# Performance work log

Hardware: AMD Instinct MI355X
Metric: run time of the kernel (lower is better)

The kernel has to match this reference:

```python
import jax, jax.numpy as jnp
import numpy as np

NEG = -9e15


def make_adj_mask(edge_index, n):
    # dense mask: 0 on edges and diagonal, -9e15 elsewhere (vectorized version of the source loop)
    A = jnp.full((n, n), NEG, dtype=jnp.float32)
    A = jnp.where(jnp.eye(n, dtype=bool), 0.0, A)
    A = A.at[edge_index[0], edge_index[1]].set(0.0)
    return A


def gat_layer(x, W, b, a_left, a_right, mask, num_heads, concat, alpha=0.2):
    n = x.shape[0]
    feats = (x @ W + b).reshape(n, num_heads, -1)           # [n, h, c]
    s_src = jnp.einsum('nhc,ch->nh', feats, a_left)          # score of source (column) node
    s_tgt = jnp.einsum('nhc,ch->nh', feats, a_right)         # score of target (row) node
    # all_scores[i, j, h] = s_src[j, h] + s_tgt[i, h]
    scores = jax.nn.leaky_relu(s_src[None, :, :] + s_tgt[:, None, :], alpha)
    scores = jnp.transpose(scores, (2, 0, 1)) + mask         # [h, n, n]
    attn = jax.nn.softmax(scores, axis=2)
    out = jnp.einsum('hij,jhc->ihc', attn, feats)            # [n, h, c]
    if concat:
        return out.reshape(n, -1)
    return out.mean(axis=1)


def setup_inputs() -> dict:
    key = jax.random.key(0)
    ks = jax.random.split(key, 10)
    N, F, H, C_HID, N_CLS, E = 4096, 512, 8, 64, 7, 65536
    c_ph = C_HID // H  # 8 per head
    s = 0.05
    return {
        'x': jax.random.normal(ks[0], (N, F), dtype=jnp.float32),
        'edge_index': jax.random.randint(ks[1], (2, E), 0, N, dtype=jnp.int32),
        'W1': jax.random.normal(ks[2], (F, C_HID), dtype=jnp.float32) * s,
        'b1': jnp.zeros((C_HID,), dtype=jnp.float32),
        'a_left1': jax.random.normal(ks[3], (c_ph, H), dtype=jnp.float32) * s,
        'a_right1': jax.random.normal(ks[4], (c_ph, H), dtype=jnp.float32) * s,
        'W2': jax.random.normal(ks[5], (C_HID, N_CLS), dtype=jnp.float32) * s,
        'b2': jnp.zeros((N_CLS,), dtype=jnp.float32),
        'a_left2': jax.random.normal(ks[6], (N_CLS, 1), dtype=jnp.float32) * s,
        'a_right2': jax.random.normal(ks[7], (N_CLS, 1), dtype=jnp.float32) * s,
    }


def reference(x, edge_index, W1, b1, a_left1, a_right1, W2, b2, a_left2, a_right2):
    n = x.shape[0]
    mask = make_adj_mask(edge_index, n)
    h1 = gat_layer(x, W1, b1, a_left1, a_right1, mask, num_heads=8, concat=True)
    h1 = jax.nn.elu(h1)
    out = gat_layer(h1, W2, b2, a_left2, a_right2, mask, num_heads=1, concat=False)
    return out
```

## Files before the change

kernel.cpp:

```cpp
#include <hip/hip_runtime.h>
#include <math.h>

#define NNODES 4096
#define WPR 128
#define FDIM 512
#define CHID 64
#define NHEAD 8
#define NCLS 7
#define MAXD 4096

typedef short bf16x8 __attribute__((ext_vector_type(8)));
typedef float f32x4  __attribute__((ext_vector_type(4)));

static __device__ inline short f2bf(float f) {
    union { float f; unsigned u; } v; v.f = f;
    unsigned r = v.u + 0x7fffu + ((v.u >> 16) & 1u);
    return (short)(r >> 16);
}

__global__ void k_init(unsigned int* __restrict__ adj, const float* __restrict__ W1,
                       short* __restrict__ Bp) {
    int bid = blockIdx.x;
    if (bid < 2048) {
        int idx = bid * 256 + threadIdx.x;
        int row = idx >> 7;
        int w = idx & (WPR - 1);
        adj[idx] = (w == (row >> 5)) ? (1u << (row & 31)) : 0u;
    } else {
        int t = (bid - 2048) * 256 + threadIdx.x;
        int j = t & 7, l = (t >> 3) & 63, w = (t >> 9) & 3, kb = t >> 11;
        Bp[t] = f2bf(W1[(kb * 32 + (l >> 4) * 8 + j) * 64 + (w * 16 + (l & 15))]);
    }
}

__global__ void k_adj_edges(const int* __restrict__ ei, unsigned int* __restrict__ adj, int E) {
    int e = blockIdx.x * blockDim.x + threadIdx.x;
    if (e >= E) return;
    int r = ei[e];
    int c = ei[E + e];
    atomicOr(&adj[r * WPR + (c >> 5)], 1u << (c & 31));
}

__global__ void __launch_bounds__(256) k_gemm1(const float* __restrict__ x, const short* __restrict__ Bp,
                                               const float* __restrict__ b, const float* __restrict__ al,
                                               const float* __restrict__ ar,
                                               const unsigned int* __restrict__ adj,
                                               float* __restrict__ feats, float* __restrict__ s1,
                                               int* __restrict__ nbrL, int* __restrict__ degA) {
    const int w = threadIdx.x >> 6, l = threadIdx.x & 63;
    const int row0 = blockIdx.x * 16;
    const int arow = row0 + (l & 15);
    const int koff = (l >> 4) * 8;
    f32x4 acc = {0.f, 0.f, 0.f, 0.f};
    const bf16x8* bp = (const bf16x8*)Bp;
    #pragma unroll
    for (int kb = 0; kb < 16; ++kb) {
        const float* ap = &x[arow * FDIM + kb * 32 + koff];
        const float4 a0 = *(const float4*)ap;
        const float4 a1 = *(const float4*)(ap + 4);
        bf16x8 af = { f2bf(a0.x), f2bf(a0.y), f2bf(a0.z), f2bf(a0.w),
                      f2bf(a1.x), f2bf(a1.y), f2bf(a1.z), f2bf(a1.w) };
        bf16x8 bfr = bp[(kb * 4 + w) * 64 + l];
        acc = __builtin_amdgcn_mfma_f32_16x16x32_bf16(af, bfr, acc, 0, 0, 0);
    }
    const int col = w * 16 + (l & 15);
    const int r0 = row0 + (l >> 4) * 4;
    const float bias = b[col];
    const int c = col & 7, h = col >> 3;
    const float vl = al[c * NHEAD + h];
    const float vr = ar[c * NHEAD + h];
    #pragma unroll
    for (int r = 0; r < 4; ++r) {
        float fv = acc[r] + bias;
        feats[(r0 + r) * CHID + col] = fv;
        float ps = fv * vl, pt = fv * vr;
        ps += __shfl_xor(ps, 1); ps += __shfl_xor(ps, 2); ps += __shfl_xor(ps, 4);
        pt += __shfl_xor(pt, 1); pt += __shfl_xor(pt, 2); pt += __shfl_xor(pt, 4);
        if ((l & 7) == 0) {
            s1[(r0 + r) * 16 + h] = ps;
            s1[(r0 + r) * 16 + 8 + h] = pt;
        }
    }
    for (int q = 0; q < 4; ++q) {
        const int i = row0 + w * 4 + q;
        const unsigned w0 = adj[i * WPR + 2 * l];
        const unsigned w1 = adj[i * WPR + 2 * l + 1];
        const int c0 = __popc(w0), c1 = __popc(w1);
        const int tot = c0 + c1;
        int v = tot;
        #pragma unroll
        for (int d = 1; d < 64; d <<= 1) {
            int t = __shfl_up(v, d);
            if (l >= d) v += t;
        }
        const int excl = v - tot;
        int base = i * MAXD + excl;
        unsigned bits = w0; int p = 0;
        while (bits) { int bb = __ffs(bits) - 1; bits &= bits - 1; nbrL[base + p++] = l * 64 + bb; }
        base += c0;
        bits = w1; p = 0;
        while (bits) { int bb = __ffs(bits) - 1; bits &= bits - 1; nbrL[base + p++] = l * 64 + 32 + bb; }
        if (l == 63) degA[i] = v;
    }
}

__global__ void __launch_bounds__(256) k_attn1(const int* __restrict__ nbrL, const int* __restrict__ degA,
                                               const float* __restrict__ feats,
                                               const float* __restrict__ s1,
                                               const float* __restrict__ W2,
                                               const float* __restrict__ b2,
                                               const float* __restrict__ al2,
                                               const float* __restrict__ ar2,
                                               float* __restrict__ feats2,
                                               float* __restrict__ s2) {
    const int w = threadIdx.x >> 6, l = threadIdx.x & 63;
    const int i = blockIdx.x * 4 + w;
    const int h = l >> 3;
    const int nn = degA[i];
    const float stgt = s1[i * 16 + 8 + h];
    float den = 0.f, acc = 0.f;
    for (int k0 = 0; k0 < nn; k0 += 64) {
        const int rem = nn - k0;
        const int cmax = rem < 64 ? rem : 64;
        const int jv = nbrL[i * MAXD + k0 + (l < cmax ? l : 0)];
        for (int k = 0; k < cmax; ++k) {
            const int j = __shfl(jv, k);
            float sc = s1[j * 16 + h] + stgt;
            sc = sc > 0.f ? sc : 0.2f * sc;
            const float p = __expf(sc);
            den += p;
            acc = fmaf(p, feats[j * CHID + l], acc);
        }
    }
    const float o = acc / den;
    const float h1v = o > 0.f ? o : (__expf(o) - 1.f);
    float t[NCLS];
    #pragma unroll
    for (int c2 = 0; c2 < NCLS; ++c2) {
        float p = h1v * W2[l * NCLS + c2];
        p += __shfl_xor(p, 1);  p += __shfl_xor(p, 2);  p += __shfl_xor(p, 4);
        p += __shfl_xor(p, 8);  p += __shfl_xor(p, 16); p += __shfl_xor(p, 32);
        t[c2] = p + b2[c2];
    }
    if (l == 0) {
        float ss = 0.f, st = 0.f;
        #pragma unroll
        for (int c2 = 0; c2 < NCLS; ++c2) {
            ss = fmaf(t[c2], al2[c2], ss);
            st = fmaf(t[c2], ar2[c2], st);
        }
        #pragma unroll
        for (int c2 = 0; c2 < NCLS; ++c2) feats2[i * 8 + c2] = t[c2];
        feats2[i * 8 + 7] = 0.f;
        s2[i * 2] = ss;
        s2[i * 2 + 1] = st;
    }
}

__global__ void __launch_bounds__(256) k_attn2(const int* __restrict__ nbrL, const int* __restrict__ degA,
                                               const float* __restrict__ feats2,
                                               const float* __restrict__ s2,
                                               float* __restrict__ out) {
    const int w = threadIdx.x >> 6, l = threadIdx.x & 63;
    const int i = blockIdx.x * 4 + w;
    const int nn = degA[i];
    const int c = l & 7;
    const float stgt = s2[i * 2 + 1];
    float den = 0.f, acc = 0.f;
    for (int k0 = 0; k0 < nn; k0 += 64) {
        const int rem = nn - k0;
        const int cmax = rem < 64 ? rem : 64;
        const int jv = nbrL[i * MAXD + k0 + (l < cmax ? l : 0)];
        for (int k = 0; k < cmax; ++k) {
            const int j = __shfl(jv, k);
            float sc = s2[j * 2] + stgt;
            sc = sc > 0.f ? sc : 0.2f * sc;
            const float p = __expf(sc);
            den += p;
            acc = fmaf(p, feats2[j * 8 + c], acc);
        }
    }
    if (l < NCLS) out[i * NCLS + l] = acc / den;
}

extern "C" void kernel_launch(void* const* d_in, const int* in_sizes, int n_in,
                              void* d_out, int out_size, void* d_ws, size_t ws_size,
                              hipStream_t stream) {
    const float* x   = (const float*)d_in[0];
    const int*   ei  = (const int*)d_in[1];
    const float* W1  = (const float*)d_in[2];
    const float* b1  = (const float*)d_in[3];
    const float* al1 = (const float*)d_in[4];
    const float* ar1 = (const float*)d_in[5];
    const float* W2  = (const float*)d_in[6];
    const float* b2  = (const float*)d_in[7];
    const float* al2 = (const float*)d_in[8];
    const float* ar2 = (const float*)d_in[9];
    float* out = (float*)d_out;
    int E = in_sizes[1] / 2;

    char* ws = (char*)d_ws;
    unsigned int* adj = (unsigned int*)ws;
    short* Bp     = (short*)(ws + (2u << 20));
    float* feats1 = (float*)(ws + (3u << 20));
    float* s1     = (float*)(ws + (4u << 20));
    float* feats2 = (float*)(ws + (5u << 20));
    float* s2     = (float*)(ws + (6u << 20));
    int*   degA   = (int*)  (ws + (7u << 20));
    int*   nbrL   = (int*)  (ws + (16u << 20));

    k_init    <<<2176, 256, 0, stream>>>(adj, W1, Bp);
    k_adj_edges<<<(E + 255) / 256, 256, 0, stream>>>(ei, adj, E);
    k_gemm1   <<<NNODES / 16, 256, 0, stream>>>(x, Bp, b1, al1, ar1, adj, feats1, s1, nbrL, degA);
    k_attn1   <<<NNODES / 4, 256, 0, stream>>>(nbrL, degA, feats1, s1, W2, b2, al2, ar2, feats2, s2);
    k_attn2   <<<NNODES / 4, 256, 0, stream>>>(nbrL, degA, feats2, s2, out);
}
```

Baseline: 114.3 us.

## Fuse all GAT stages into one cooperative persistent kernel with grid syncs

Replaces the five separate launches with a single cooperative kernel that runs init, edge scatter, neighbor-list build, GEMM, and both attention layers in sequence, separated by grid-wide barriers. Work is distributed with grid-stride loops over a grid sized from occupancy (up to 4 blocks per CU), and the neighbor-list build is split from the GEMM. This removes per-launch overhead and inter-kernel gaps. In exchange it adds grid.sync costs and a fixed grid size that may load-balance less well than the original launches. It also adds a fast path for nodes with at most 64 neighbors.

Measured after the change: 344.6 us. 3.02x slower.

```diff
diff --git a/kernel.cpp b/kernel.cpp
--- a/kernel.cpp
+++ b/kernel.cpp
@@ -1,5 +1,8 @@
 #include <hip/hip_runtime.h>
+#include <hip/hip_cooperative_groups.h>
 #include <math.h>
+
+namespace cg = cooperative_groups;
 
 #define NNODES 4096
 #define WPR 128
@@ -18,71 +21,44 @@
     return (short)(r >> 16);
 }
 
-__global__ void k_init(unsigned int* __restrict__ adj, const float* __restrict__ W1,
-                       short* __restrict__ Bp) {
-    int bid = blockIdx.x;
-    if (bid < 2048) {
-        int idx = bid * 256 + threadIdx.x;
-        int row = idx >> 7;
-        int w = idx & (WPR - 1);
-        adj[idx] = (w == (row >> 5)) ? (1u << (row & 31)) : 0u;
-    } else {
-        int t = (bid - 2048) * 256 + threadIdx.x;
-        int j = t & 7, l = (t >> 3) & 63, w = (t >> 9) & 3, kb = t >> 11;
-        Bp[t] = f2bf(W1[(kb * 32 + (l >> 4) * 8 + j) * 64 + (w * 16 + (l & 15))]);
-    }
-}
-
-__global__ void k_adj_edges(const int* __restrict__ ei, unsigned int* __restrict__ adj, int E) {
-    int e = blockIdx.x * blockDim.x + threadIdx.x;
-    if (e >= E) return;
-    int r = ei[e];
-    int c = ei[E + e];
-    atomicOr(&adj[r * WPR + (c >> 5)], 1u << (c & 31));
-}
-
-__global__ void __launch_bounds__(256) k_gemm1(const float* __restrict__ x, const short* __restrict__ Bp,
-                                               const float* __restrict__ b, const float* __restrict__ al,
-                                               const float* __restrict__ ar,
-                                               const unsigned int* __restrict__ adj,
-                                               float* __restrict__ feats, float* __restrict__ s1,
-                                               int* __restrict__ nbrL, int* __restrict__ degA) {
-    const int w = threadIdx.x >> 6, l = threadIdx.x & 63;
-    const int row0 = blockIdx.x * 16;
-    const int arow = row0 + (l & 15);
-    const int koff = (l >> 4) * 8;
-    f32x4 acc = {0.f, 0.f, 0.f, 0.f};
-    const bf16x8* bp = (const bf16x8*)Bp;
-    #pragma unroll
-    for (int kb = 0; kb < 16; ++kb) {
-        const float* ap = &x[arow * FDIM + kb * 32 + koff];
-        const float4 a0 = *(const float4*)ap;
-        const float4 a1 = *(const float4*)(ap + 4);
-        bf16x8 af = { f2bf(a0.x), f2bf(a0.y), f2bf(a0.z), f2bf(a0.w),
-                      f2bf(a1.x), f2bf(a1.y), f2bf(a1.z), f2bf(a1.w) };
-        bf16x8 bfr = bp[(kb * 4 + w) * 64 + l];
-        acc = __builtin_amdgcn_mfma_f32_16x16x32_bf16(af, bfr, acc, 0, 0, 0);
-    }
-    const int col = w * 16 + (l & 15);
-    const int r0 = row0 + (l >> 4) * 4;
-    const float bias = b[col];
-    const int c = col & 7, h = col >> 3;
-    const float vl = al[c * NHEAD + h];
-    const float vr = ar[c * NHEAD + h];
-    #pragma unroll
-    for (int r = 0; r < 4; ++r) {
-        float fv = acc[r] + bias;
-        feats[(r0 + r) * CHID + col] = fv;
-        float ps = fv * vl, pt = fv * vr;
-        ps += __shfl_xor(ps, 1); ps += __shfl_xor(ps, 2); ps += __shfl_xor(ps, 4);
-        pt += __shfl_xor(pt, 1); pt += __shfl_xor(pt, 2); pt += __shfl_xor(pt, 4);
-        if ((l & 7) == 0) {
-            s1[(r0 + r) * 16 + h] = ps;
-            s1[(r0 + r) * 16 + 8 + h] = pt;
-        }
-    }
-    for (int q = 0; q < 4; ++q) {
-        const int i = row0 + w * 4 + q;
+__global__ void __launch_bounds__(256, 4)
+k_fused(const float* __restrict__ x, const int* __restrict__ ei,
+        const float* __restrict__ W1, const float* __restrict__ b1,
+        const float* __restrict__ al1, const float* __restrict__ ar1,
+        const float* __restrict__ W2, const float* __restrict__ b2,
+        const float* __restrict__ al2, const float* __restrict__ ar2,
+        float* __restrict__ out, int E,
+        unsigned int* __restrict__ adj, short* __restrict__ Bp,
+        float* __restrict__ feats1, float* __restrict__ s1,
+        float* __restrict__ feats2, float* __restrict__ s2,
+        int* __restrict__ nbrL, int* __restrict__ degA) {
+    cg::grid_group grid = cg::this_grid();
+    const int tid = threadIdx.x, bid = blockIdx.x;
+    const int w = tid >> 6, l = tid & 63;
+    const int gw = bid * 4 + w;
+    const int gid = bid * 256 + tid;
+    const int nwaves = gridDim.x * 4;
+    const int gstride = gridDim.x * 256;
+
+    for (int i = gw; i < NNODES; i += nwaves) {
+        const int d = i >> 5;
+        const unsigned bit = 1u << (i & 31);
+        adj[i * WPR + l]      = (l == d)        ? bit : 0u;
+        adj[i * WPR + 64 + l] = ((64 + l) == d) ? bit : 0u;
+    }
+    for (int t = gid; t < 32768; t += gstride) {
+        int j = t & 7, ll = (t >> 3) & 63, ww = (t >> 9) & 3, kb = t >> 11;
+        Bp[t] = f2bf(W1[(kb * 32 + (ll >> 4) * 8 + j) * 64 + (ww * 16 + (ll & 15))]);
+    }
+    grid.sync();
+
+    for (int e = gid; e < E; e += gstride) {
+        int r = ei[e], c = ei[E + e];
+        atomicOr(&adj[r * WPR + (c >> 5)], 1u << (c & 31));
+    }
+    grid.sync();
+
+    for (int i = gw; i < NNODES; i += nwaves) {
         const unsigned w0 = adj[i * WPR + 2 * l];
         const unsigned w1 = adj[i * WPR + 2 * l + 1];
         const int c0 = __popc(w0), c1 = __popc(w1);
@@ -93,8 +69,7 @@
             int t = __shfl_up(v, d);
             if (l >= d) v += t;
         }
-        const int excl = v - tot;
-        int base = i * MAXD + excl;
+        int base = i * MAXD + (v - tot);
         unsigned bits = w0; int p = 0;
         while (bits) { int bb = __ffs(bits) - 1; bits &= bits - 1; nbrL[base + p++] = l * 64 + bb; }
         base += c0;
@@ -102,85 +77,137 @@
         while (bits) { int bb = __ffs(bits) - 1; bits &= bits - 1; nbrL[base + p++] = l * 64 + 32 + bb; }
         if (l == 63) degA[i] = v;
     }
-}
-
-__global__ void __launch_bounds__(256) k_attn1(const int* __restrict__ nbrL, const int* __restrict__ degA,
-                                               const float* __restrict__ feats,
-                                               const float* __restrict__ s1,
-                                               const float* __restrict__ W2,
-                                               const float* __restrict__ b2,
-                                               const float* __restrict__ al2,
-                                               const float* __restrict__ ar2,
-                                               float* __restrict__ feats2,
-                                               float* __restrict__ s2) {
-    const int w = threadIdx.x >> 6, l = threadIdx.x & 63;
-    const int i = blockIdx.x * 4 + w;
-    const int h = l >> 3;
-    const int nn = degA[i];
-    const float stgt = s1[i * 16 + 8 + h];
-    float den = 0.f, acc = 0.f;
-    for (int k0 = 0; k0 < nn; k0 += 64) {
-        const int rem = nn - k0;
-        const int cmax = rem < 64 ? rem : 64;
-        const int jv = nbrL[i * MAXD + k0 + (l < cmax ? l : 0)];
-        for (int k = 0; k < cmax; ++k) {
-            const int j = __shfl(jv, k);
-            float sc = s1[j * 16 + h] + stgt;
-            sc = sc > 0.f ? sc : 0.2f * sc;
-            const float p = __expf(sc);
-            den += p;
-            acc = fmaf(p, feats[j * CHID + l], acc);
-        }
-    }
-    const float o = acc / den;
-    const float h1v = o > 0.f ? o : (__expf(o) - 1.f);
-    float t[NCLS];
-    #pragma unroll
-    for (int c2 = 0; c2 < NCLS; ++c2) {
-        float p = h1v * W2[l * NCLS + c2];
-        p += __shfl_xor(p, 1);  p += __shfl_xor(p, 2);  p += __shfl_xor(p, 4);
-        p += __shfl_xor(p, 8);  p += __shfl_xor(p, 16); p += __shfl_xor(p, 32);
-        t[c2] = p + b2[c2];
-    }
-    if (l == 0) {
-        float ss = 0.f, st = 0.f;
-        #pragma unroll
-        for (int c2 = 0; c2 < NCLS; ++c2) {
-            ss = fmaf(t[c2], al2[c2], ss);
-            st = fmaf(t[c2], ar2[c2], st);
-        }
-        #pragma unroll
-        for (int c2 = 0; c2 < NCLS; ++c2) feats2[i * 8 + c2] = t[c2];
-        feats2[i * 8 + 7] = 0.f;
-        s2[i * 2] = ss;
-        s2[i * 2 + 1] = st;
-    }
-}
-
-__global__ void __launch_bounds__(256) k_attn2(const int* __restrict__ nbrL, const int* __restrict__ degA,
-                                               const float* __restrict__ feats2,
-                                               const float* __restrict__ s2,
-                                               float* __restrict__ out) {
-    const int w = threadIdx.x >> 6, l = threadIdx.x & 63;
-    const int i = blockIdx.x * 4 + w;
-    const int nn = degA[i];
-    const int c = l & 7;
-    const float stgt = s2[i * 2 + 1];
-    float den = 0.f, acc = 0.f;
-    for (int k0 = 0; k0 < nn; k0 += 64) {
-        const int rem = nn - k0;
-        const int cmax = rem < 64 ? rem : 64;
-        const int jv = nbrL[i * MAXD + k0 + (l < cmax ? l : 0)];
-        for (int k = 0; k < cmax; ++k) {
-            const int j = __shfl(jv, k);
-            float sc = s2[j * 2] + stgt;
-            sc = sc > 0.f ? sc : 0.2f * sc;
-            const float p = __expf(sc);
-            den += p;
-            acc = fmaf(p, feats2[j * 8 + c], acc);
-        }
-    }
-    if (l < NCLS) out[i * NCLS + l] = acc / den;
+    {
+        const bf16x8* bp = (const bf16x8*)Bp;
+        for (int tb = bid; tb < NNODES / 16; tb += gridDim.x) {
+            const int row0 = tb * 16;
+            const int arow = row0 + (l & 15);
+            const int koff = (l >> 4) * 8;
+            f32x4 acc = {0.f, 0.f, 0.f, 0.f};
+            #pragma unroll 4
+            for (int kb = 0; kb < 16; ++kb) {
+                const float* ap = &x[arow * FDIM + kb * 32 + koff];
+                const float4 a0 = *(const float4*)ap;
+                const float4 a1 = *(const float4*)(ap + 4);
+                bf16x8 af = { f2bf(a0.x), f2bf(a0.y), f2bf(a0.z), f2bf(a0.w),
+                              f2bf(a1.x), f2bf(a1.y), f2bf(a1.z), f2bf(a1.w) };
+                bf16x8 bfr = bp[(kb * 4 + w) * 64 + l];
+                acc = __builtin_amdgcn_mfma_f32_16x16x32_bf16(af, bfr, acc, 0, 0, 0);
+            }
+            const int col = w * 16 + (l & 15);
+            const int r0 = row0 + (l >> 4) * 4;
+            const float bias = b1[col];
+            const int c = col & 7, h = col >> 3;
+            const float vl = al1[c * NHEAD + h];
+            const float vr = ar1[c * NHEAD + h];
+            #pragma unroll
+            for (int r = 0; r < 4; ++r) {
+                float fv = acc[r] + bias;
+                feats1[(r0 + r) * CHID + col] = fv;
+                float ps = fv * vl, pt = fv * vr;
+                ps += __shfl_xor(ps, 1); ps += __shfl_xor(ps, 2); ps += __shfl_xor(ps, 4);
+                pt += __shfl_xor(pt, 1); pt += __shfl_xor(pt, 2); pt += __shfl_xor(pt, 4);
+                if ((l & 7) == 0) {
+                    s1[(r0 + r) * 16 + h] = ps;
+                    s1[(r0 + r) * 16 + 8 + h] = pt;
+                }
+            }
+        }
+    }
+    grid.sync();
+
+    {
+        const int h = l >> 3;
+        for (int i = gw; i < NNODES; i += nwaves) {
+            const int nn = degA[i];
+            const float stgt = s1[i * 16 + 8 + h];
+            float den = 0.f, acc = 0.f;
+            if (nn <= 64) {
+                const int jv = nbrL[i * MAXD + l];
+                for (int k = 0; k < nn; ++k) {
+                    const int j = __shfl(jv, k);
+                    float sc = s1[j * 16 + h] + stgt;
+                    sc = sc > 0.f ? sc : 0.2f * sc;
+                    const float p = __expf(sc);
+                    den += p;
+                    acc = fmaf(p, feats1[j * CHID + l], acc);
+                }
+            } else {
+                for (int k0 = 0; k0 < nn; k0 += 64) {
+                    const int rem = nn - k0;
+                    const int cmax = rem < 64 ? rem : 64;
+                    const int jv = nbrL[i * MAXD + k0 + (l < cmax ? l : 0)];
+                    for (int k = 0; k < cmax; ++k) {
+                        const int j = __shfl(jv, k);
+                        float sc = s1[j * 16 + h] + stgt;
+                        sc = sc > 0.f ? sc : 0.2f * sc;
+                        const float p = __expf(sc);
+                        den += p;
+                        acc = fmaf(p, feats1[j * CHID + l], acc);
+                    }
+                }
+            }
+            const float o = acc / den;
+            const float h1v = o > 0.f ? o : (__expf(o) - 1.f);
+            float t7[NCLS];
+            #pragma unroll
+            for (int c2 = 0; c2 < NCLS; ++c2) {
+                float p = h1v * W2[l * NCLS + c2];
+                p += __shfl_xor(p, 1);  p += __shfl_xor(p, 2);  p += __shfl_xor(p, 4);
+                p += __shfl_xor(p, 8);  p += __shfl_xor(p, 16); p += __shfl_xor(p, 32);
+                t7[c2] = p + b2[c2];
+            }
+            if (l == 0) {
+                float ss = 0.f, st = 0.f;
+                #pragma unroll
+                for (int c2 = 0; c2 < NCLS; ++c2) {
+                    ss = fmaf(t7[c2], al2[c2], ss);
+                    st = fmaf(t7[c2], ar2[c2], st);
+                }
+                #pragma unroll
+                for (int c2 = 0; c2 < NCLS; ++c2) feats2[i * 8 + c2] = t7[c2];
+                feats2[i * 8 + 7] = 0.f;
+                s2[i * 2] = ss;
+                s2[i * 2 + 1] = st;
+            }
+        }
+    }
+    grid.sync();
+
+    {
+        const int c = l & 7;
+        for (int i = gw; i < NNODES; i += nwaves) {
+            const int nn = degA[i];
+            const float stgt = s2[i * 2 + 1];
+            float den = 0.f, acc = 0.f;
+            if (nn <= 64) {
+                const int jv = nbrL[i * MAXD + l];
+                for (int k = 0; k < nn; ++k) {
+                    const int j = __shfl(jv, k);
+                    float sc = s2[j * 2] + stgt;
+                    sc = sc > 0.f ? sc : 0.2f * sc;
+                    const float p = __expf(sc);
+                    den += p;
+                    acc = fmaf(p, feats2[j * 8 + c], acc);
+                }
+            } else {
+                for (int k0 = 0; k0 < nn; k0 += 64) {
+                    const int rem = nn - k0;
+                    const int cmax = rem < 64 ? rem : 64;
+                    const int jv = nbrL[i * MAXD + k0 + (l < cmax ? l : 0)];
+                    for (int k = 0; k < cmax; ++k) {
+                        const int j = __shfl(jv, k);
+                        float sc = s2[j * 2] + stgt;
+                        sc = sc > 0.f ? sc : 0.2f * sc;
+                        const float p = __expf(sc);
+                        den += p;
+                        acc = fmaf(p, feats2[j * 8 + c], acc);
+                    }
+                }
+            }
+            if (l < NCLS) out[i * NCLS + l] = acc / den;
+        }
+    }
 }
 
 extern "C" void kernel_launch(void* const* d_in, const int* in_sizes, int n_in,
@@ -209,9 +236,15 @@
     int*   degA   = (int*)  (ws + (7u << 20));
     int*   nbrL   = (int*)  (ws + (16u << 20));
 
-    k_init    <<<2176, 256, 0, stream>>>(adj, W1, Bp);
-    k_adj_edges<<<(E + 255) / 256, 256, 0, stream>>>(ei, adj, E);
-    k_gemm1   <<<NNODES / 16, 256, 0, stream>>>(x, Bp, b1, al1, ar1, adj, feats1, s1, nbrL, degA);
-    k_attn1   <<<NNODES / 4, 256, 0, stream>>>(nbrL, degA, feats1, s1, W2, b2, al2, ar2, feats2, s2);
-    k_attn2   <<<NNODES / 4, 256, 0, stream>>>(nbrL, degA, feats2, s2, out);
+    int nb = 0;
+    hipError_t oerr = hipOccupancyMaxActiveBlocksPerMultiprocessor(&nb, k_fused, 256, 0);
+    if (oerr != hipSuccess || nb < 1) nb = 1;
+    if (nb > 4) nb = 4;
+    dim3 gridDim(256 * nb), blockDim(256);
+
+    void* args[] = { (void*)&x, (void*)&ei, (void*)&W1, (void*)&b1, (void*)&al1, (void*)&ar1,
+                     (void*)&W2, (void*)&b2, (void*)&al2, (void*)&ar2, (void*)&out, (void*)&E,
+                     (void*)&adj, (void*)&Bp, (void*)&feats1, (void*)&s1,
+                     (void*)&feats2, (void*)&s2, (void*)&nbrL, (void*)&degA };
+    hipLaunchCooperativeKernel((void*)k_fused, gridDim, blockDim, args, 0, stream);
 }
```

## Build neighbor lists via atomic scatter and split GEMM K across waves

Applied to the files above, without the earlier changes.

Neighbor lists are now built directly in the edge scatter kernel: the first setter of each adjacency bit claims a slot with an atomicAdd on the row degree, and self-loops are added as extra edges. This replaces the per-row bitmap scan, prefix sum and compaction that the GEMM kernel used to do. The GEMM now splits the K dimension across the four waves, each computing all 64 columns, and reduces the partial sums through shared memory. The attention kernels gain a fast path for rows with at most 64 neighbors. Neighbor order becomes nondeterministic, which can slightly change float summation order.

Measured after the change: 110.5 us. -3.3%, faster.

```diff
diff --git a/kernel.cpp b/kernel.cpp
--- a/kernel.cpp
+++ b/kernel.cpp
@@ -18,60 +18,74 @@
     return (short)(r >> 16);
 }
 
-__global__ void k_init(unsigned int* __restrict__ adj, const float* __restrict__ W1,
-                       short* __restrict__ Bp) {
-    int bid = blockIdx.x;
-    if (bid < 2048) {
-        int idx = bid * 256 + threadIdx.x;
-        int row = idx >> 7;
-        int w = idx & (WPR - 1);
-        adj[idx] = (w == (row >> 5)) ? (1u << (row & 31)) : 0u;
-    } else {
-        int t = (bid - 2048) * 256 + threadIdx.x;
-        int j = t & 7, l = (t >> 3) & 63, w = (t >> 9) & 3, kb = t >> 11;
-        Bp[t] = f2bf(W1[(kb * 32 + (l >> 4) * 8 + j) * 64 + (w * 16 + (l & 15))]);
-    }
-}
-
-__global__ void k_adj_edges(const int* __restrict__ ei, unsigned int* __restrict__ adj, int E) {
-    int e = blockIdx.x * blockDim.x + threadIdx.x;
-    if (e >= E) return;
-    int r = ei[e];
-    int c = ei[E + e];
-    atomicOr(&adj[r * WPR + (c >> 5)], 1u << (c & 31));
-}
-
-__global__ void __launch_bounds__(256) k_gemm1(const float* __restrict__ x, const short* __restrict__ Bp,
-                                               const float* __restrict__ b, const float* __restrict__ al,
-                                               const float* __restrict__ ar,
-                                               const unsigned int* __restrict__ adj,
-                                               float* __restrict__ feats, float* __restrict__ s1,
-                                               int* __restrict__ nbrL, int* __restrict__ degA) {
+__global__ void k_init(unsigned int* __restrict__ adj, int* __restrict__ deg,
+                       const float* __restrict__ W1, short* __restrict__ Bp) {
+    const int gid = blockIdx.x * 256 + threadIdx.x;
+    const int gs = gridDim.x * 256;
+    for (int t = gid; t < NNODES * WPR; t += gs) adj[t] = 0u;
+    for (int t = gid; t < NNODES; t += gs) deg[t] = 0;
+    for (int t = gid; t < 32768; t += gs) {
+        int j = t & 7, l = (t >> 3) & 63, cq = (t >> 9) & 3, kb = t >> 11;
+        Bp[t] = f2bf(W1[(kb * 32 + (l >> 4) * 8 + j) * 64 + (cq * 16 + (l & 15))]);
+    }
+}
+
+__global__ void k_scatter(const int* __restrict__ ei, int E, unsigned int* __restrict__ adj,
+                          int* __restrict__ deg, int* __restrict__ nbrL) {
+    const int t = blockIdx.x * 256 + threadIdx.x;
+    if (t >= E + NNODES) return;
+    int r, c;
+    if (t < E) { r = ei[t]; c = ei[E + t]; }
+    else       { r = c = t - E; }
+    const unsigned bit = 1u << (c & 31);
+    const unsigned old = atomicOr(&adj[r * WPR + (c >> 5)], bit);
+    if (!(old & bit)) {
+        const int p = atomicAdd(&deg[r], 1);
+        nbrL[r * MAXD + p] = c;
+    }
+}
+
+__global__ void __launch_bounds__(256) k_gemm(const float* __restrict__ x, const short* __restrict__ Bp,
+                                              const float* __restrict__ b1, const float* __restrict__ al,
+                                              const float* __restrict__ ar,
+                                              float* __restrict__ feats, float* __restrict__ s1) {
+    __shared__ float red[4][4][64][4];
     const int w = threadIdx.x >> 6, l = threadIdx.x & 63;
     const int row0 = blockIdx.x * 16;
     const int arow = row0 + (l & 15);
     const int koff = (l >> 4) * 8;
-    f32x4 acc = {0.f, 0.f, 0.f, 0.f};
     const bf16x8* bp = (const bf16x8*)Bp;
-    #pragma unroll
-    for (int kb = 0; kb < 16; ++kb) {
+    f32x4 acc0 = {0,0,0,0}, acc1 = {0,0,0,0}, acc2 = {0,0,0,0}, acc3 = {0,0,0,0};
+    #pragma unroll
+    for (int q = 0; q < 4; ++q) {
+        const int kb = w * 4 + q;
         const float* ap = &x[arow * FDIM + kb * 32 + koff];
         const float4 a0 = *(const float4*)ap;
         const float4 a1 = *(const float4*)(ap + 4);
         bf16x8 af = { f2bf(a0.x), f2bf(a0.y), f2bf(a0.z), f2bf(a0.w),
                       f2bf(a1.x), f2bf(a1.y), f2bf(a1.z), f2bf(a1.w) };
-        bf16x8 bfr = bp[(kb * 4 + w) * 64 + l];
-        acc = __builtin_amdgcn_mfma_f32_16x16x32_bf16(af, bfr, acc, 0, 0, 0);
-    }
+        acc0 = __builtin_amdgcn_mfma_f32_16x16x32_bf16(af, bp[(kb * 4 + 0) * 64 + l], acc0, 0, 0, 0);
+        acc1 = __builtin_amdgcn_mfma_f32_16x16x32_bf16(af, bp[(kb * 4 + 1) * 64 + l], acc1, 0, 0, 0);
+        acc2 = __builtin_amdgcn_mfma_f32_16x16x32_bf16(af, bp[(kb * 4 + 2) * 64 + l], acc2, 0, 0, 0);
+        acc3 = __builtin_amdgcn_mfma_f32_16x16x32_bf16(af, bp[(kb * 4 + 3) * 64 + l], acc3, 0, 0, 0);
+    }
+    #pragma unroll
+    for (int r = 0; r < 4; ++r) {
+        red[w][0][l][r] = acc0[r];
+        red[w][1][l][r] = acc1[r];
+        red[w][2][l][r] = acc2[r];
+        red[w][3][l][r] = acc3[r];
+    }
+    __syncthreads();
     const int col = w * 16 + (l & 15);
     const int r0 = row0 + (l >> 4) * 4;
-    const float bias = b[col];
+    const float bias = b1[col];
     const int c = col & 7, h = col >> 3;
     const float vl = al[c * NHEAD + h];
     const float vr = ar[c * NHEAD + h];
     #pragma unroll
     for (int r = 0; r < 4; ++r) {
-        float fv = acc[r] + bias;
+        float fv = red[0][w][l][r] + red[1][w][l][r] + red[2][w][l][r] + red[3][w][l][r] + bias;
         feats[(r0 + r) * CHID + col] = fv;
         float ps = fv * vl, pt = fv * vr;
         ps += __shfl_xor(ps, 1); ps += __shfl_xor(ps, 2); ps += __shfl_xor(ps, 4);
@@ -81,30 +95,9 @@
             s1[(r0 + r) * 16 + 8 + h] = pt;
         }
     }
-    for (int q = 0; q < 4; ++q) {
-        const int i = row0 + w * 4 + q;
-        const unsigned w0 = adj[i * WPR + 2 * l];
-        const unsigned w1 = adj[i * WPR + 2 * l + 1];
-        const int c0 = __popc(w0), c1 = __popc(w1);
-        const int tot = c0 + c1;
-        int v = tot;
-        #pragma unroll
-        for (int d = 1; d < 64; d <<= 1) {
-            int t = __shfl_up(v, d);
-            if (l >= d) v += t;
-        }
-        const int excl = v - tot;
-        int base = i * MAXD + excl;
-        unsigned bits = w0; int p = 0;
-        while (bits) { int bb = __ffs(bits) - 1; bits &= bits - 1; nbrL[base + p++] = l * 64 + bb; }
-        base += c0;
-        bits = w1; p = 0;
-        while (bits) { int bb = __ffs(bits) - 1; bits &= bits - 1; nbrL[base + p++] = l * 64 + 32 + bb; }
-        if (l == 63) degA[i] = v;
-    }
-}
-
-__global__ void __launch_bounds__(256) k_attn1(const int* __restrict__ nbrL, const int* __restrict__ degA,
+}
+
+__global__ void __launch_bounds__(256) k_attn1(const int* __restrict__ nbrL, const int* __restrict__ deg,
                                                const float* __restrict__ feats,
                                                const float* __restrict__ s1,
                                                const float* __restrict__ W2,
@@ -116,14 +109,12 @@
     const int w = threadIdx.x >> 6, l = threadIdx.x & 63;
     const int i = blockIdx.x * 4 + w;
     const int h = l >> 3;
-    const int nn = degA[i];
+    const int nn = deg[i];
     const float stgt = s1[i * 16 + 8 + h];
     float den = 0.f, acc = 0.f;
-    for (int k0 = 0; k0 < nn; k0 += 64) {
-        const int rem = nn - k0;
-        const int cmax = rem < 64 ? rem : 64;
-        const int jv = nbrL[i * MAXD + k0 + (l < cmax ? l : 0)];
-        for (int k = 0; k < cmax; ++k) {
+    if (nn <= 64) {
+        const int jv = nbrL[i * MAXD + (l < nn ? l : 0)];
+        for (int k = 0; k < nn; ++k) {
             const int j = __shfl(jv, k);
             float sc = s1[j * 16 + h] + stgt;
             sc = sc > 0.f ? sc : 0.2f * sc;
@@ -131,53 +122,79 @@
             den += p;
             acc = fmaf(p, feats[j * CHID + l], acc);
         }
+    } else {
+        for (int k0 = 0; k0 < nn; k0 += 64) {
+            const int rem = nn - k0;
+            const int cmax = rem < 64 ? rem : 64;
+            const int jv = nbrL[i * MAXD + k0 + (l < cmax ? l : 0)];
+            for (int k = 0; k < cmax; ++k) {
+                const int j = __shfl(jv, k);
+                float sc = s1[j * 16 + h] + stgt;
+                sc = sc > 0.f ? sc : 0.2f * sc;
+                const float p = __expf(sc);
+                den += p;
+                acc = fmaf(p, feats[j * CHID + l], acc);
+            }
+        }
     }
     const float o = acc / den;
     const float h1v = o > 0.f ? o : (__expf(o) - 1.f);
-    float t[NCLS];
+    float t7[NCLS];
     #pragma unroll
     for (int c2 = 0; c2 < NCLS; ++c2) {
         float p = h1v * W2[l * NCLS + c2];
         p += __shfl_xor(p, 1);  p += __shfl_xor(p, 2);  p += __shfl_xor(p, 4);
         p += __shfl_xor(p, 8);  p += __shfl_xor(p, 16); p += __shfl_xor(p, 32);
-        t[c2] = p + b2[c2];
+        t7[c2] = p + b2[c2];
     }
     if (l == 0) {
         float ss = 0.f, st = 0.f;
         #pragma unroll
         for (int c2 = 0; c2 < NCLS; ++c2) {
-            ss = fmaf(t[c2], al2[c2], ss);
-            st = fmaf(t[c2], ar2[c2], st);
+            ss = fmaf(t7[c2], al2[c2], ss);
+            st = fmaf(t7[c2], ar2[c2], st);
         }
         #pragma unroll
-        for (int c2 = 0; c2 < NCLS; ++c2) feats2[i * 8 + c2] = t[c2];
+        for (int c2 = 0; c2 < NCLS; ++c2) feats2[i * 8 + c2] = t7[c2];
         feats2[i * 8 + 7] = 0.f;
         s2[i * 2] = ss;
         s2[i * 2 + 1] = st;
     }
 }
 
-__global__ void __launch_bounds__(256) k_attn2(const int* __restrict__ nbrL, const int* __restrict__ degA,
+__global__ void __launch_bounds__(256) k_attn2(const int* __restrict__ nbrL, const int* __restrict__ deg,
                                                const float* __restrict__ feats2,
                                                const float* __restrict__ s2,
                                                float* __restrict__ out) {
     const int w = threadIdx.x >> 6, l = threadIdx.x & 63;
     const int i = blockIdx.x * 4 + w;
-    const int nn = degA[i];
+    const int nn = deg[i];
     const int c = l & 7;
     const float stgt = s2[i * 2 + 1];
     float den = 0.f, acc = 0.f;
-    for (int k0 = 0; k0 < nn; k0 += 64) {
-        const int rem = nn - k0;
-        const int cmax = rem < 64 ? rem : 64;
-        const int jv = nbrL[i * MAXD + k0 + (l < cmax ? l : 0)];
-        for (int k = 0; k < cmax; ++k) {
+    if (nn <= 64) {
+        const int jv = nbrL[i * MAXD + (l < nn ? l : 0)];
+        for (int k = 0; k < nn; ++k) {
             const int j = __shfl(jv, k);
             float sc = s2[j * 2] + stgt;
             sc = sc > 0.f ? sc : 0.2f * sc;
             const float p = __expf(sc);
             den += p;
             acc = fmaf(p, feats2[j * 8 + c], acc);
+        }
+    } else {
+        for (int k0 = 0; k0 < nn; k0 += 64) {
+            const int rem = nn - k0;
+            const int cmax = rem < 64 ? rem : 64;
+            const int jv = nbrL[i * MAXD + k0 + (l < cmax ? l : 0)];
+            for (int k = 0; k < cmax; ++k) {
+                const int j = __shfl(jv, k);
+                float sc = s2[j * 2] + stgt;
+                sc = sc > 0.f ? sc : 0.2f * sc;
+                const float p = __expf(sc);
+                den += p;
+                acc = fmaf(p, feats2[j * 8 + c], acc);
+            }
         }
     }
     if (l < NCLS) out[i * NCLS + l] = acc / den;
@@ -206,12 +223,12 @@
     float* s1     = (float*)(ws + (4u << 20));
     float* feats2 = (float*)(ws + (5u << 20));
     float* s2     = (float*)(ws + (6u << 20));
-    int*   degA   = (int*)  (ws + (7u << 20));
+    int*   deg    = (int*)  (ws + (7u << 20));
     int*   nbrL   = (int*)  (ws + (16u << 20));
 
-    k_init    <<<2176, 256, 0, stream>>>(adj, W1, Bp);
-    k_adj_edges<<<(E + 255) / 256, 256, 0, stream>>>(ei, adj, E);
-    k_gemm1   <<<NNODES / 16, 256, 0, stream>>>(x, Bp, b1, al1, ar1, adj, feats1, s1, nbrL, degA);
-    k_attn1   <<<NNODES / 4, 256, 0, stream>>>(nbrL, degA, feats1, s1, W2, b2, al2, ar2, feats2, s2);
-    k_attn2   <<<NNODES / 4, 256, 0, stream>>>(nbrL, degA, feats2, s2, out);
-}
+    k_init   <<<2048, 256, 0, stream>>>(adj, deg, W1, Bp);
+    k_scatter<<<(E + NNODES + 255) / 256, 256, 0, stream>>>(ei, E, adj, deg, nbrL);
+    k_gemm   <<<NNODES / 16, 256, 0, stream>>>(x, Bp, b1, al1, ar1, feats1, s1);
+    k_attn1  <<<NNODES / 4, 256, 0, stream>>>(nbrL, deg, feats1, s1, W2, b2, al2, ar2, feats2, s2);
+    k_attn2  <<<NNODES / 4, 256, 0, stream>>>(nbrL, deg, feats2, s2, out);
+}
```
